# Kernel tuning notes

Measured on AMD Instinct MI355X. Metric: run time of the kernel, lower is better.

The kernel has to match this reference:

```python
import jax, jax.numpy as jnp
import numpy as np

# Config derived from init_kwargs
DIM = 256
DSTATE = 64
DCONV = 3
HEADDIM = 64
CHUNK = 256
NGROUPS = 1
DINNER = int(2.0 * DIM)                 # 512
NHEADS = DINNER // HEADDIM              # 8
CONVDIM = DINNER + 2 * NGROUPS * DSTATE  # 640 (x, B, C share the depthwise conv)
DPROJ = 2 * DINNER + 2 * NGROUPS * DSTATE + NHEADS  # z + xBC + dt


def setup_inputs() -> dict:
    key = jax.random.key(0)
    ks = jax.random.split(key, 8)
    B, H, W = 8, 64, 64
    return dict(
        x=jax.random.normal(ks[0], (B, DIM, H, W), jnp.float32),
        ln_w=jnp.ones((DIM,), jnp.float32),
        ln_b=jnp.zeros((DIM,), jnp.float32),
        in_proj_w=jax.random.normal(ks[1], (DPROJ, DIM), jnp.float32) * 0.02,
        conv_w=jax.random.normal(ks[2], (CONVDIM, 1, DCONV, DCONV), jnp.float32) * 0.1,
        conv_b=jnp.zeros((CONVDIM,), jnp.float32),
        A_log=jnp.log(jax.random.uniform(ks[3], (NHEADS,), jnp.float32, 1.0, 16.0)),
        D=jnp.ones((NHEADS,), jnp.float32),
        dt_bias=jax.random.uniform(ks[4], (NHEADS,), jnp.float32, -2.0, 0.0),
        rms_w=jnp.ones((DINNER,), jnp.float32),
        out_proj_w=jax.random.normal(ks[5], (DIM, DINNER), jnp.float32) * 0.02,
    )


def _ssd(X, dA, Bm, Cm, chunk):
    """Mamba2 SSD chunked parallel scan.
    X:  (b, l, h, p)  inputs already multiplied by dt
    dA: (b, l, h)     dt * A (negative)
    Bm, Cm: (b, l, h, n)
    """
    b, l, h, p = X.shape
    n = Bm.shape[-1]
    c = l // chunk
    q = chunk
    Xc = X.reshape(b, c, q, h, p)
    Bc = Bm.reshape(b, c, q, h, n)
    Cc = Cm.reshape(b, c, q, h, n)
    Ac = dA.reshape(b, c, q, h).transpose(0, 3, 1, 2)            # (b,h,c,q)
    Acs = jnp.cumsum(Ac, axis=-1)                                # (b,h,c,q)
    # intra-chunk (diagonal blocks): causal decay matrix L
    tri = jnp.tril(jnp.ones((q, q), bool))
    Ldec = jnp.where(tri, jnp.exp(Acs[..., :, None] - Acs[..., None, :]), 0.0)
    Y_diag = jnp.einsum('bcqhn,bcshn,bhcqs,bcshp->bcqhp', Cc, Bc, Ldec, Xc)
    # per-chunk final states
    decay_states = jnp.exp(Acs[..., -1:] - Acs)                  # (b,h,c,q)
    states = jnp.einsum('bcqhn,bhcq,bcqhp->bchpn', Bc, decay_states, Xc)
    # inter-chunk recurrence (segment-sum over chunk totals)
    A_last = jnp.pad(Acs[..., -1], ((0, 0), (0, 0), (1, 0)))     # (b,h,c+1)
    ccs = jnp.cumsum(A_last, axis=-1)
    tric = jnp.tril(jnp.ones((c + 1, c + 1), bool))
    decay_chunk = jnp.where(tric, jnp.exp(ccs[..., :, None] - ccs[..., None, :]), 0.0)
    states0 = jnp.concatenate([jnp.zeros_like(states[:, :1]), states], axis=1)
    prev = jnp.einsum('bhzc,bchpn->bzhpn', decay_chunk, states0)[:, :-1]
    # contribution of carried-in state (off-diagonal blocks)
    Y_off = jnp.einsum('bcqhn,bchpn,bhcq->bcqhp', Cc, prev, jnp.exp(Acs))
    return (Y_diag + Y_off).reshape(b, l, h, p)


def _forward(x, ln_w, ln_b, in_proj_w, conv_w, conv_b, A_log, D, dt_bias, rms_w, out_proj_w):
    Bn, Cd, Hh, Ww = x.shape
    L = Hh * Ww
    # LayerNorm over channel dim (channel-first LayerNorm2d)
    mu = jnp.mean(x, axis=1, keepdims=True)
    var = jnp.mean((x - mu) ** 2, axis=1, keepdims=True)
    xn = (x - mu) * jax.lax.rsqrt(var + 1e-5)
    xn = xn * ln_w[None, :, None, None] + ln_b[None, :, None, None]
    # input projection (1x1): -> z | xBC | dt
    zxbcdt = jnp.einsum('bchw,dc->bdhw', xn, in_proj_w)
    z = zxbcdt[:, :DINNER]
    xBC = zxbcdt[:, DINNER:DINNER + CONVDIM]
    dt = zxbcdt[:, DINNER + CONVDIM:]                            # (b, nheads, H, W)
    # depthwise 2D conv + SiLU on xBC
    xBC = jax.lax.conv_general_dilated(
        xBC, conv_w, (1, 1), 'SAME',
        dimension_numbers=('NCHW', 'OIHW', 'NCHW'), feature_group_count=CONVDIM)
    xBC = jax.nn.silu(xBC + conv_b[None, :, None, None])
    # flatten spatial -> sequence, channel-last
    def to_seq(t):
        return t.reshape(Bn, t.shape[1], L).transpose(0, 2, 1)
    xBC, dt, z = to_seq(xBC), to_seq(dt), to_seq(z)
    xs = xBC[..., :DINNER].reshape(Bn, L, NHEADS, HEADDIM)
    Bg = xBC[..., DINNER:DINNER + NGROUPS * DSTATE].reshape(Bn, L, NGROUPS, DSTATE)
    Cg = xBC[..., DINNER + NGROUPS * DSTATE:].reshape(Bn, L, NGROUPS, DSTATE)
    hpg = NHEADS // NGROUPS
    Bm = jnp.repeat(Bg, hpg, axis=2)
    Cm = jnp.repeat(Cg, hpg, axis=2)
    dt = jax.nn.softplus(dt + dt_bias[None, None, :])            # (b, L, nheads)
    A = -jnp.exp(A_log)
    y = _ssd(xs * dt[..., None], dt * A[None, None, :], Bm, Cm, CHUNK)
    y = y + D[None, None, :, None] * xs                          # skip connection
    y = y.reshape(Bn, L, DINNER)
    # gated RMSNorm: norm(y * silu(z)) * w
    y = y * jax.nn.silu(z)
    y = y * jax.lax.rsqrt(jnp.mean(y * y, axis=-1, keepdims=True) + 1e-5) * rms_w
    out = jnp.einsum('bld,cd->blc', y, out_proj_w)
    out = out.transpose(0, 2, 1).reshape(Bn, Cd, Hh, Ww)
    return x + out                                               # residual


def reference(x, ln_w, ln_b, in_proj_w, conv_w, conv_b, A_log, D, dt_bias, rms_w, out_proj_w):
    return _forward(x, ln_w, ln_b, in_proj_w, conv_w, conv_b, A_log, D, dt_bias, rms_w, out_proj_w)
```

## Files before the change

### kernel.cpp

```cpp
#include <hip/hip_runtime.h>
#include <hip/hip_bf16.h>
#include <math.h>

#define DIMC   256
#define LSP    4096
#define BATCH  8
#define DINNER 512
#define NHEADS 8
#define HEADDIM 64
#define DSTATE 64
#define CONVDIM 640
#define DPROJ  1160
#define MPAD   1280
#define CHUNK  256
#define NCHUNK 16

typedef unsigned short u16;
typedef __attribute__((ext_vector_type(8))) unsigned short u16x8;
typedef __attribute__((ext_vector_type(8))) short s16x8;
typedef __attribute__((ext_vector_type(4))) float f32x4;

#define MFMA16(a,b,c) __builtin_amdgcn_mfma_f32_16x16x32_bf16((s16x8)(a),(s16x8)(b),(c),0,0,0)

__device__ __forceinline__ float bf2f(u16 u){ return __uint_as_float(((unsigned int)u)<<16); }
__device__ __forceinline__ u16 f2bf(float f){
  unsigned int x = __float_as_uint(f);
  unsigned int r = (x + 0x7fffu + ((x>>16)&1u)) >> 16;
  return (u16)r;
}
__device__ __forceinline__ float softplusf(float x){ return (x > 20.f) ? x : log1pf(expf(x)); }
__device__ __forceinline__ float siluf(float x){ return x / (1.f + expf(-x)); }

__global__ void convert_w(const float* __restrict__ src, u16* __restrict__ dst,
                          int total, int valid){
  int i = blockIdx.x*256 + threadIdx.x;
  if (i >= total) return;
  dst[i] = (i < valid) ? f2bf(src[i]) : (u16)0;
}

__global__ void convert_w_rms(const float* __restrict__ src, const float* __restrict__ rmsw,
                              u16* __restrict__ dst){
  int i = blockIdx.x*256 + threadIdx.x;
  if (i >= DIMC*DINNER) return;
  dst[i] = f2bf(src[i] * rmsw[i & (DINNER-1)]);
}

__global__ void ln_kernel(const float* __restrict__ X, const float* __restrict__ lnw,
                          const float* __restrict__ lnb, u16* __restrict__ XNT) {
  int pos = blockIdx.x*256 + threadIdx.x;
  int b = pos >> 12, l = pos & (LSP-1);
  const float* xb = X + ((size_t)b*DIMC)*LSP + l;
  float sum=0.f, sq=0.f;
  for (int c=0;c<DIMC;c++){ float v=xb[(size_t)c*LSP]; sum+=v; sq+=v*v; }
  float mu = sum*(1.f/DIMC);
  float var = sq*(1.f/DIMC) - mu*mu;
  float rs = rsqrtf(var + 1e-5f);
  u16* ob = XNT + ((size_t)(b*LSP + l))*DIMC;
  for (int c0=0;c0<DIMC;c0+=8){
    u16x8 v8;
    #pragma unroll
    for(int j=0;j<8;j++){
      float v = xb[(size_t)(c0+j)*LSP];
      v8[j] = f2bf((v-mu)*rs*lnw[c0+j] + lnb[c0+j]);
    }
    *(u16x8*)&ob[c0] = v8;
  }
}

__global__ __launch_bounds__(256,2) void gemm_in_fused(
    const u16* __restrict__ W, const u16* __restrict__ XNT,
    u16* __restrict__ ZT, u16* __restrict__ XBC, u16* __restrict__ DT){
  __shared__ u16 Xs[128][264];
  __shared__ u16 Ws[128][32];
  int tid=threadIdx.x, w=tid>>6, lane=tid&63, l15=lane&15, quad=lane>>4;
  int n0=blockIdx.x*128, mh=blockIdx.y, b=blockIdx.z;
  {
    const u16* src = XNT + ((size_t)(b*LSP + n0))*DIMC;
    #pragma unroll
    for (int i=0;i<16;i++){
      int g = i*256 + tid;
      int row = g>>5, c8 = (g&31)*8;
      *(u16x8*)&Xs[row][c8] = *(const u16x8*)&src[(size_t)row*DIMC + c8];
    }
  }
  for (int pti=0; pti<5; pti++){
    int ptg = mh*5 + pti;
    int m0 = ptg*128;
    f32x4 acc[4][4];
    #pragma unroll
    for(int i=0;i<4;i++)
      #pragma unroll
      for(int j=0;j<4;j++) acc[i][j]=(f32x4){0.f,0.f,0.f,0.f};
    for (int k0=0;k0<DIMC;k0+=32){
      __syncthreads();
      {
        int ch = tid*2;
        int r = ch>>2, o=(ch&3)*8;
        *(u16x8*)&Ws[r][o] = *(const u16x8*)&W[(size_t)(m0+r)*DIMC + k0 + o];
        ch++; r = ch>>2; o=(ch&3)*8;
        *(u16x8*)&Ws[r][o] = *(const u16x8*)&W[(size_t)(m0+r)*DIMC + k0 + o];
      }
      __syncthreads();
      u16x8 af[4], bfr[4];
      if (ptg < 4){
        #pragma unroll
        for(int mt=0;mt<4;mt++) af[mt] = *(const u16x8*)&Xs[(w>>1)*64+mt*16+l15][k0+quad*8];
        #pragma unroll
        for(int nt=0;nt<4;nt++) bfr[nt] = *(const u16x8*)&Ws[(w&1)*64+nt*16+l15][quad*8];
      } else {
        #pragma unroll
        for(int mt=0;mt<4;mt++) af[mt] = *(const u16x8*)&Ws[(w>>1)*64+mt*16+l15][quad*8];
        #pragma unroll
        for(int nt=0;nt<4;nt++) bfr[nt] = *(const u16x8*)&Xs[(w&1)*64+nt*16+l15][k0+quad*8];
      }
      #pragma unroll
      for(int mt=0;mt<4;mt++)
        #pragma unroll
        for(int nt=0;nt<4;nt++)
          acc[mt][nt]=MFMA16(af[mt],bfr[nt],acc[mt][nt]);
    }
    if (ptg < 4){
      #pragma unroll
      for(int mt=0;mt<4;mt++)
        #pragma unroll
        for(int nt=0;nt<4;nt++)
          #pragma unroll
          for(int r=0;r<4;r++){
            int lrow = n0 + (w>>1)*64 + mt*16 + quad*4 + r;
            int dcol = m0 + (w&1)*64 + nt*16 + l15;
            ZT[((size_t)b*LSP + lrow)*DINNER + dcol] = f2bf(acc[mt][nt][r]);
          }
    } else {
      #pragma unroll
      for(int mt=0;mt<4;mt++)
        #pragma unroll
        for(int nt=0;nt<4;nt++)
          #pragma unroll
          for(int r=0;r<4;r++){
            int prow = m0 + (w>>1)*64 + mt*16 + quad*4 + r;
            if (prow>=DPROJ) continue;
            int col = n0 + (w&1)*64 + nt*16 + l15;
            u16 v = f2bf(acc[mt][nt][r]);
            if (prow<DINNER+CONVDIM)  XBC[((size_t)b*CONVDIM+(prow-DINNER))*LSP+col]=v;
            else                      DT[((size_t)b*NHEADS+(prow-DINNER-CONVDIM))*LSP+col]=v;
          }
    }
  }
}

__global__ void gemm_out_mfma(const u16* __restrict__ A, const u16* __restrict__ Bm,
                              const float* __restrict__ Res, float* __restrict__ Out){
  __shared__ u16 As[128][32];
  __shared__ u16 Bs[128][32];
  __shared__ float rinv[128];
  int tid=threadIdx.x, w=tid>>6, lane=tid&63, l15=lane&15, quad=lane>>4;
  int b=blockIdx.z, m0=blockIdx.y*128, n0=blockIdx.x*128;
  const u16* Bb = Bm + ((size_t)b*LSP + n0)*DINNER;
  for (int rr=w; rr<128; rr+=4){
    u16x8 v = *(const u16x8*)&Bb[(size_t)rr*DINNER + lane*8];
    float s=0.f;
    #pragma unroll
    for(int j=0;j<8;j++){ float f=bf2f(v[j]); s+=f*f; }
    #pragma unroll
    for(int o=32;o>0;o>>=1) s += __shfl_xor(s,o,64);
    if (lane==0) rinv[rr] = rsqrtf(s*(1.f/DINNER) + 1e-5f);
  }
  f32x4 acc[4][4];
  #pragma unroll
  for(int i=0;i<4;i++)
    #pragma unroll
    for(int j=0;j<4;j++) acc[i][j] = (f32x4){0.f,0.f,0.f,0.f};
  for (int k0=0;k0<DINNER;k0+=32){
    __syncthreads();
    {
      int ch = tid*2;
      int r = ch>>2, o=(ch&3)*8;
      *(u16x8*)&As[r][o] = *(const u16x8*)&A[(size_t)(m0+r)*DINNER + k0 + o];
      *(u16x8*)&Bs[r][o] = *(const u16x8*)&Bb[(size_t)r*DINNER + k0 + o];
      ch++; r = ch>>2; o=(ch&3)*8;
      *(u16x8*)&As[r][o] = *(const u16x8*)&A[(size_t)(m0+r)*DINNER + k0 + o];
      *(u16x8*)&Bs[r][o] = *(const u16x8*)&Bb[(size_t)r*DINNER + k0 + o];
    }
    __syncthreads();
    u16x8 af[4], bfr[4];
    #pragma unroll
    for(int mt=0;mt<4;mt++) af[mt] = *(const u16x8*)&As[(w>>1)*64+mt*16+l15][quad*8];
    #pragma unroll
    for(int nt=0;nt<4;nt++) bfr[nt] = *(const u16x8*)&Bs[(w&1)*64+nt*16+l15][quad*8];
    #pragma unroll
    for(int mt=0;mt<4;mt++)
      #pragma unroll
      for(int nt=0;nt<4;nt++)
        acc[mt][nt]=MFMA16(af[mt],bfr[nt],acc[mt][nt]);
  }
  #pragma unroll
  for(int mt=0;mt<4;mt++)
    #pragma unroll
    for(int nt=0;nt<4;nt++){
      float rv = rinv[(w&1)*64 + nt*16 + l15];
      #pragma unroll
      for(int r=0;r<4;r++){
        int row = m0 + (w>>1)*64 + mt*16 + quad*4 + r;
        int col = n0 + (w&1)*64 + nt*16 + l15;
        size_t oi = ((size_t)b*DIMC+row)*LSP+col;
        Out[oi] = acc[mt][nt][r]*rv + Res[oi];
      }
    }
}

__global__ void conv_kernel(u16* __restrict__ XBC, const float* __restrict__ CW,
                            const float* __restrict__ CB){
  int ch = blockIdx.x, b = blockIdx.y, tid = threadIdx.x;
  __shared__ float plane[66*66];
  u16* base = XBC + ((size_t)b*CONVDIM + ch)*LSP;
  for (int idx=tid; idx<66*66; idx+=256){
    int yy = idx/66 - 1, xx = idx%66 - 1;
    float v = 0.f;
    if (yy>=0 && yy<64 && xx>=0 && xx<64) v = bf2f(base[yy*64+xx]);
    plane[idx] = v;
  }
  float wg[9];
  #pragma unroll
  for (int t=0;t<9;t++) wg[t] = CW[ch*9+t];
  float bias = CB[ch];
  __syncthreads();
  for (int r=0;r<16;r++){
    int pix = tid + r*256;
    int y = pix>>6, x = pix&63;
    float s=0.f;
    #pragma unroll
    for(int dy=0;dy<3;dy++)
      #pragma unroll
      for(int dx=0;dx<3;dx++) s += plane[(y+dy)*66 + x+dx]*wg[dy*3+dx];
    base[pix] = f2bf(siluf(s + bias));
  }
}

__global__ void ssd_pre_kernel(const u16* __restrict__ DT, const float* __restrict__ A_log,
                               const float* __restrict__ dt_bias, float* __restrict__ ACS,
                               float* __restrict__ DTV, float* __restrict__ DASUM){
  int c=blockIdx.x, h=blockIdx.y, b=blockIdx.z, tid=threadIdx.x;
  __shared__ float acs[CHUNK];
  size_t base = ((size_t)b*NHEADS+h)*LSP + c*CHUNK + tid;
  float raw = bf2f(DT[base]);
  float dtv = softplusf(raw + dt_bias[h]);
  float Ah = -expf(A_log[h]);
  acs[tid] = dtv*Ah;
  __syncthreads();
  for(int o=1;o<256;o<<=1){
    float add=(tid>=o)?acs[tid-o]:0.f;
    __syncthreads(); acs[tid]+=add; __syncthreads();
  }
  ACS[base] = acs[tid];
  DTV[base] = dtv;
  if (tid==CHUNK-1) DASUM[((size_t)b*NHEADS+h)*NCHUNK+c] = acs[tid];
}

__global__ __launch_bounds__(256,4) void ssd_states_mfma(
    const float* __restrict__ ACS, const float* __restrict__ DTV,
    const float* __restrict__ DASUM, const u16* __restrict__ XBC,
    float* __restrict__ STATES){
  int c=blockIdx.x, h=blockIdx.y, b=blockIdx.z;
  int tid=threadIdx.x, w=tid>>6, lane=tid&63, l15=lane&15, quad=lane>>4;
  __shared__ float wdt[CHUNK];
  __shared__ u16 Xw[64][136];
  __shared__ u16 Bn[64][136];
  {
    size_t base = ((size_t)b*NHEADS+h)*LSP + c*CHUNK + tid;
    float atot = DASUM[((size_t)b*NHEADS+h)*NCHUNK+c];
    wdt[tid] = DTV[base]*expf(atot - ACS[base]);
  }
  __syncthreads();
  f32x4 acc[4];
  #pragma unroll
  for(int i=0;i<4;i++) acc[i] = (f32x4){0.f,0.f,0.f,0.f};
  size_t cb = (size_t)c*CHUNK;
  for(int th=0; th<2; th++){
    __syncthreads();
    {
      int n=tid&63, q4=tid>>6;
      const u16* Xg = XBC + ((size_t)b*CONVDIM + h*HEADDIM + n)*LSP + cb + th*128;
      const u16* Bg = XBC + ((size_t)b*CONVDIM + DINNER + n)*LSP + cb + th*128;
      #pragma unroll
      for(int i=0;i<4;i++){
        int o = q4*32+i*8;
        u16x8 v = *(const u16x8*)&Xg[o];
        u16x8 wv;
        #pragma unroll
        for(int j=0;j<8;j++) wv[j]=f2bf(bf2f(v[j])*wdt[th*128+o+j]);
        *(u16x8*)&Xw[n][o]=wv;
        *(u16x8*)&Bn[n][o] = *(const u16x8*)&Bg[o];
      }
    }
    __syncthreads();
    #pragma unroll
    for(int k8=0;k8<4;k8++){
      u16x8 a = *(const u16x8*)&Xw[w*16+l15][k8*32+quad*8];
      #pragma unroll
      for(int nt=0;nt<4;nt++){
        u16x8 bb = *(const u16x8*)&Bn[nt*16+l15][k8*32+quad*8];
        acc[nt]=MFMA16(a,bb,acc[nt]);
      }
    }
  }
  float* dst = STATES + (((size_t)b*NHEADS+h)*NCHUNK+c)*4096;
  #pragma unroll
  for(int nt=0;nt<4;nt++)
    #pragma unroll
    for(int r=0;r<4;r++)
      dst[(w*16+quad*4+r)*64 + nt*16+l15] = acc[nt][r];
}

__global__ void ssd_scan_kernel(const float* __restrict__ STATES, const float* __restrict__ DASUM,
                                u16* __restrict__ PREVB){
  int g = blockIdx.x, h = blockIdx.y, b = blockIdx.z, tid = threadIdx.x;
  int e = g*256 + tid;
  size_t hb = (size_t)b*NHEADS + h;
  size_t base = hb*NCHUNK*4096 + e;
  float s = 0.f;
  for (int cc=0;cc<NCHUNK;cc++){
    PREVB[base + (size_t)cc*4096] = f2bf(s);
    s = s*expf(DASUM[hb*NCHUNK + cc]) + STATES[base + (size_t)cc*4096];
  }
}

__global__ __launch_bounds__(256,4) void ssd_y_mfma(
    const float* __restrict__ ACS, const float* __restrict__ DTV,
    const u16* __restrict__ XBC, const float* __restrict__ Dp,
    const u16* __restrict__ PREVB, const u16* __restrict__ ZT,
    u16* __restrict__ YG){
  int bx = blockIdx.x; int c = bx>>2, tb = bx&3;
  int h = blockIdx.y, b = blockIdx.z;
  int tid=threadIdx.x, w=tid>>6, lane=tid&63, l15=lane&15, quad=lane>>4;
  __shared__ float acs[CHUNK];
  __shared__ float dtv[CHUNK];
  __shared__ u16 Ct[64][72];
  __shared__ u16 Bsb[64][72];
  __shared__ u16 Xsb[64][72];
  __shared__ u16 P[4][16][72];
  {
    size_t base = ((size_t)b*NHEADS+h)*LSP + c*CHUNK + tid;
    acs[tid] = ACS[base];
    dtv[tid] = DTV[base];
  }
  {
    int n = tid&63, q4 = tid>>6;
    const u16* Cg = XBC + ((size_t)b*CONVDIM + DINNER + DSTATE + n)*LSP + (size_t)c*CHUNK + tb*64;
    #pragma unroll
    for(int i=0;i<2;i++){
      u16x8 v = *(const u16x8*)&Cg[q4*16+i*8];
      #pragma unroll
      for(int j=0;j<8;j++) Ct[q4*16+i*8+j][n]=v[j];
    }
  }
  __syncthreads();
  f32x4 Yd[4], Yo[4];
  #pragma unroll
  for(int i=0;i<4;i++){ Yd[i]=(f32x4){0.f,0.f,0.f,0.f}; Yo[i]=(f32x4){0.f,0.f,0.f,0.f}; }
  int trow = w*16 + l15;
  u16x8 ca0 = *(const u16x8*)&Ct[trow][quad*8];
  u16x8 ca1 = *(const u16x8*)&Ct[trow][32+quad*8];
  {
    const u16* Pg = PREVB + (((size_t)b*NHEADS+h)*NCHUNK + c)*4096;
    #pragma unroll
    for(int pt=0;pt<4;pt++){
      u16x8 b0 = *(const u16x8*)&Pg[(pt*16+l15)*64 + quad*8];
      u16x8 b1 = *(const u16x8*)&Pg[(pt*16+l15)*64 + 32 + quad*8];
      Yo[pt]=MFMA16(ca0,b0,Yo[pt]);
      Yo[pt]=MFMA16(ca1,b1,Yo[pt]);
    }
  }
  int tloc = tb*64 + w*16 + quad*4;
  float acst[4];
  #pragma unroll
  for(int r=0;r<4;r++) acst[r] = acs[tloc+r];
  for(int sb=0; sb<=tb; sb++){
    __syncthreads();
    {
      int n=tid&63, q4=tid>>6;
      const u16* Bg = XBC + ((size_t)b*CONVDIM + DINNER + n)*LSP + (size_t)c*CHUNK + sb*64;
      #pragma unroll
      for(int i=0;i<2;i++){
        u16x8 v = *(const u16x8*)&Bg[q4*16+i*8];
        #pragma unroll
        for(int j=0;j<8;j++) Bsb[q4*16+i*8+j][n]=v[j];
      }
      const u16* Xg = XBC + ((size_t)b*CONVDIM + h*HEADDIM + n)*LSP + (size_t)c*CHUNK + sb*64;
      #pragma unroll
      for(int i=0;i<2;i++){
        int o = q4*16+i*8;
        *(u16x8*)&Xsb[n][o] = *(const u16x8*)&Xg[o];
      }
    }
    __syncthreads();
    f32x4 S[4];
    #pragma unroll
    for(int st=0;st<4;st++) S[st]=(f32x4){0.f,0.f,0.f,0.f};
    #pragma unroll
    for(int st=0;st<4;st++){
      u16x8 b0 = *(const u16x8*)&Bsb[st*16+l15][quad*8];
      u16x8 b1 = *(const u16x8*)&Bsb[st*16+l15][32+quad*8];
      S[st]=MFMA16(ca0,b0,S[st]);
      S[st]=MFMA16(ca1,b1,S[st]);
    }
    if (sb < tb){
      #pragma unroll
      for(int st=0;st<4;st++){
        int s = sb*64 + st*16 + l15;
        float as = acs[s];
        float dv = dtv[s];
        #pragma unroll
        for(int r=0;r<4;r++)
          P[w][quad*4+r][st*16+l15] = f2bf(S[st][r]*expf(acst[r]-as)*dv);
      }
    } else {
      #pragma unroll
      for(int st=0;st<4;st++){
        int s = sb*64 + st*16 + l15;
        float as = acs[s];
        float dv = dtv[s];
        #pragma unroll
        for(int r=0;r<4;r++){
          float e = (s <= tloc+r) ? expf(acst[r]-as) : 0.f;
          P[w][quad*4+r][st*16+l15] = f2bf(S[st][r]*e*dv);
        }
      }
    }
    u16x8 p0 = *(const u16x8*)&P[w][l15][quad*8];
    u16x8 p1 = *(const u16x8*)&P[w][l15][32+quad*8];
    #pragma unroll
    for(int pt=0;pt<4;pt++){
      u16x8 x0 = *(const u16x8*)&Xsb[pt*16+l15][quad*8];
      u16x8 x1 = *(const u16x8*)&Xsb[pt*16+l15][32+quad*8];
      Yd[pt]=MFMA16(p0,x0,Yd[pt]);
      Yd[pt]=MFMA16(p1,x1,Yd[pt]);
    }
  }
  float Dh = Dp[h];
  float eat[4];
  #pragma unroll
  for(int r=0;r<4;r++) eat[r] = expf(acst[r]);
  size_t lbase = (size_t)b*LSP + c*CHUNK + tb*64;
  #pragma unroll
  for(int pt=0;pt<4;pt++){
    #pragma unroll
    for(int r=0;r<4;r++){
      int tl = w*16 + quad*4 + r;
      int p = pt*16 + l15;
      float xs = bf2f(Xsb[p][tl]);
      float y = Yd[pt][r] + eat[r]*Yo[pt][r] + Dh*xs;
      size_t oi = (lbase + tl)*DINNER + h*HEADDIM + p;
      float zv = bf2f(ZT[oi]);
      YG[oi] = f2bf(y * siluf(zv));
    }
  }
}

extern "C" void kernel_launch(void* const* d_in, const int* in_sizes, int n_in,
                              void* d_out, int out_size, void* d_ws, size_t ws_size,
                              hipStream_t stream) {
  const float* x     = (const float*)d_in[0];
  const float* lnw   = (const float*)d_in[1];
  const float* lnb   = (const float*)d_in[2];
  const float* inpw  = (const float*)d_in[3];
  const float* convw = (const float*)d_in[4];
  const float* convb = (const float*)d_in[5];
  const float* alog  = (const float*)d_in[6];
  const float* Dp    = (const float*)d_in[7];
  const float* dtbi  = (const float*)d_in[8];
  const float* rmsw  = (const float*)d_in[9];
  const float* outw  = (const float*)d_in[10];
  float* out = (float*)d_out;

  char* ws = (char*)d_ws;
  size_t off = 0;
  auto alloc = [&](size_t bytes)->void*{ void* p = ws+off; off += (bytes+255)&~(size_t)255; return p; };
  u16*   WPIN   = (u16*)  alloc((size_t)MPAD*DIMC*2);
  u16*   WPOUT  = (u16*)  alloc((size_t)DIMC*DINNER*2);
  char*  RA     = (char*) alloc((size_t)BATCH*NHEADS*NCHUNK*4096*4);
  u16*   XNT    = (u16*)RA;
  float* STATES = (float*)RA;
  u16*   ZT     = (u16*)  alloc((size_t)BATCH*LSP*DINNER*2);
  u16*   XBC    = (u16*)  alloc((size_t)BATCH*CONVDIM*LSP*2);
  u16*   DTb    = (u16*)  alloc((size_t)BATCH*NHEADS*LSP*2);
  u16*   PREVB  = (u16*)  alloc((size_t)BATCH*NHEADS*NCHUNK*4096*2);
  float* DASUM  = (float*)alloc((size_t)BATCH*NHEADS*NCHUNK*4);
  float* ACS    = (float*)alloc((size_t)BATCH*NHEADS*LSP*4);
  float* DTV    = (float*)alloc((size_t)BATCH*NHEADS*LSP*4);
  u16*   YG     = (u16*)  alloc((size_t)BATCH*LSP*DINNER*2);

  convert_w<<<(MPAD*DIMC+255)/256,256,0,stream>>>(inpw, WPIN, MPAD*DIMC, DPROJ*DIMC);
  convert_w_rms<<<(DIMC*DINNER+255)/256,256,0,stream>>>(outw, rmsw, WPOUT);
  ln_kernel<<<dim3(BATCH*LSP/256),256,0,stream>>>(x,lnw,lnb,XNT);
  gemm_in_fused<<<dim3(LSP/128,2,BATCH),256,0,stream>>>(WPIN, XNT, ZT, XBC, DTb);
  conv_kernel<<<dim3(CONVDIM,BATCH),256,0,stream>>>(XBC, convw, convb);
  ssd_pre_kernel<<<dim3(NCHUNK,NHEADS,BATCH),256,0,stream>>>(DTb, alog, dtbi, ACS, DTV, DASUM);
  ssd_states_mfma<<<dim3(NCHUNK,NHEADS,BATCH),256,0,stream>>>(ACS,DTV,DASUM,XBC,STATES);
  ssd_scan_kernel<<<dim3(16,NHEADS,BATCH),256,0,stream>>>(STATES,DASUM,PREVB);
  ssd_y_mfma<<<dim3(NCHUNK*4,NHEADS,BATCH),256,0,stream>>>(ACS,DTV,XBC,Dp,PREVB,ZT,YG);
  gemm_out_mfma<<<dim3(LSP/128,DIMC/128,BATCH),256,0,stream>>>(WPOUT, YG, x, out);
}
```

Baseline: 366.0 us.

## Process whole chunk per block in SSD output kernel and use fast math intrinsics

Restructures ssd_y_mfma so that one block handles a full 256-step chunk instead of one 64-row tile. Each B/X sub-block is now loaded once and reused across all later target tiles, rather than being reloaded by every tile block. The D skip term is folded into the diagonal of the decay matrix, and the inter-chunk term is computed by pre-scaling C with exp(acs) into the same accumulators. Softplus, silu and exp now use fast intrinsics (__expf, __logf, rcp). In exchange the kernel launches four times fewer blocks, needs more registers (launch bounds relaxed to 2) and more LDS, and the fast math plus the bf16 pre-scaling reduce precision.

New measurement: 376.2 us. +2.8%, slower.

```diff
diff --git a/kernel.cpp b/kernel.cpp
--- a/kernel.cpp
+++ b/kernel.cpp
@@ -28,8 +28,14 @@
   unsigned int r = (x + 0x7fffu + ((x>>16)&1u)) >> 16;
   return (u16)r;
 }
-__device__ __forceinline__ float softplusf(float x){ return (x > 20.f) ? x : log1pf(expf(x)); }
-__device__ __forceinline__ float siluf(float x){ return x / (1.f + expf(-x)); }
+__device__ __forceinline__ float softplusf(float x){ return (x > 20.f) ? x : __logf(1.f + __expf(x)); }
+__device__ __forceinline__ float siluf(float x){ return x * __builtin_amdgcn_rcpf(1.f + __expf(-x)); }
+__device__ __forceinline__ u16x8 fscale(u16x8 v, float s){
+  u16x8 r;
+  #pragma unroll
+  for(int j=0;j<8;j++) r[j] = f2bf(bf2f(v[j])*s);
+  return r;
+}
 
 __global__ void convert_w(const float* __restrict__ src, u16* __restrict__ dst,
                           int total, int valid){
@@ -244,7 +250,7 @@
   size_t base = ((size_t)b*NHEADS+h)*LSP + c*CHUNK + tid;
   float raw = bf2f(DT[base]);
   float dtv = softplusf(raw + dt_bias[h]);
-  float Ah = -expf(A_log[h]);
+  float Ah = -__expf(A_log[h]);
   acs[tid] = dtv*Ah;
   __syncthreads();
   for(int o=1;o<256;o<<=1){
@@ -268,7 +274,7 @@
   {
     size_t base = ((size_t)b*NHEADS+h)*LSP + c*CHUNK + tid;
     float atot = DASUM[((size_t)b*NHEADS+h)*NCHUNK+c];
-    wdt[tid] = DTV[base]*expf(atot - ACS[base]);
+    wdt[tid] = DTV[base]*__expf(atot - ACS[base]);
   }
   __syncthreads();
   f32x4 acc[4];
@@ -320,21 +326,20 @@
   float s = 0.f;
   for (int cc=0;cc<NCHUNK;cc++){
     PREVB[base + (size_t)cc*4096] = f2bf(s);
-    s = s*expf(DASUM[hb*NCHUNK + cc]) + STATES[base + (size_t)cc*4096];
-  }
-}
-
-__global__ __launch_bounds__(256,4) void ssd_y_mfma(
+    s = s*__expf(DASUM[hb*NCHUNK + cc]) + STATES[base + (size_t)cc*4096];
+  }
+}
+
+__global__ __launch_bounds__(256,2) void ssd_y_mfma(
     const float* __restrict__ ACS, const float* __restrict__ DTV,
     const u16* __restrict__ XBC, const float* __restrict__ Dp,
     const u16* __restrict__ PREVB, const u16* __restrict__ ZT,
     u16* __restrict__ YG){
-  int bx = blockIdx.x; int c = bx>>2, tb = bx&3;
-  int h = blockIdx.y, b = blockIdx.z;
+  int c = blockIdx.x, h = blockIdx.y, b = blockIdx.z;
   int tid=threadIdx.x, w=tid>>6, lane=tid&63, l15=lane&15, quad=lane>>4;
   __shared__ float acs[CHUNK];
   __shared__ float dtv[CHUNK];
-  __shared__ u16 Ct[64][72];
+  __shared__ u16 Ct[256][72];
   __shared__ u16 Bsb[64][72];
   __shared__ u16 Xsb[64][72];
   __shared__ u16 P[4][16][72];
@@ -345,36 +350,44 @@
   }
   {
     int n = tid&63, q4 = tid>>6;
-    const u16* Cg = XBC + ((size_t)b*CONVDIM + DINNER + DSTATE + n)*LSP + (size_t)c*CHUNK + tb*64;
-    #pragma unroll
-    for(int i=0;i<2;i++){
-      u16x8 v = *(const u16x8*)&Cg[q4*16+i*8];
-      #pragma unroll
-      for(int j=0;j<8;j++) Ct[q4*16+i*8+j][n]=v[j];
+    const u16* Cg = XBC + ((size_t)b*CONVDIM + DINNER + DSTATE + n)*LSP + (size_t)c*CHUNK + q4*64;
+    #pragma unroll
+    for(int i=0;i<8;i++){
+      u16x8 v = *(const u16x8*)&Cg[i*8];
+      #pragma unroll
+      for(int j=0;j<8;j++) Ct[q4*64+i*8+j][n]=v[j];
     }
   }
   __syncthreads();
-  f32x4 Yd[4], Yo[4];
-  #pragma unroll
-  for(int i=0;i<4;i++){ Yd[i]=(f32x4){0.f,0.f,0.f,0.f}; Yo[i]=(f32x4){0.f,0.f,0.f,0.f}; }
-  int trow = w*16 + l15;
-  u16x8 ca0 = *(const u16x8*)&Ct[trow][quad*8];
-  u16x8 ca1 = *(const u16x8*)&Ct[trow][32+quad*8];
+  f32x4 Yd[4][4];
+  #pragma unroll
+  for(int t=0;t<4;t++)
+    #pragma unroll
+    for(int p=0;p<4;p++) Yd[t][p]=(f32x4){0.f,0.f,0.f,0.f};
   {
     const u16* Pg = PREVB + (((size_t)b*NHEADS+h)*NCHUNK + c)*4096;
+    u16x8 pb0[4], pb1[4];
     #pragma unroll
     for(int pt=0;pt<4;pt++){
-      u16x8 b0 = *(const u16x8*)&Pg[(pt*16+l15)*64 + quad*8];
-      u16x8 b1 = *(const u16x8*)&Pg[(pt*16+l15)*64 + 32 + quad*8];
-      Yo[pt]=MFMA16(ca0,b0,Yo[pt]);
-      Yo[pt]=MFMA16(ca1,b1,Yo[pt]);
-    }
-  }
-  int tloc = tb*64 + w*16 + quad*4;
-  float acst[4];
-  #pragma unroll
-  for(int r=0;r<4;r++) acst[r] = acs[tloc+r];
-  for(int sb=0; sb<=tb; sb++){
+      pb0[pt] = *(const u16x8*)&Pg[(pt*16+l15)*64 + quad*8];
+      pb1[pt] = *(const u16x8*)&Pg[(pt*16+l15)*64 + 32 + quad*8];
+    }
+    #pragma unroll
+    for(int tb=0;tb<4;tb++){
+      int trow = tb*64 + w*16 + l15;
+      float ea = __expf(acs[trow]);
+      u16x8 a0 = fscale(*(const u16x8*)&Ct[trow][quad*8], ea);
+      u16x8 a1 = fscale(*(const u16x8*)&Ct[trow][32+quad*8], ea);
+      #pragma unroll
+      for(int pt=0;pt<4;pt++){
+        Yd[tb][pt]=MFMA16(a0,pb0[pt],Yd[tb][pt]);
+        Yd[tb][pt]=MFMA16(a1,pb1[pt],Yd[tb][pt]);
+      }
+    }
+  }
+  float Dh = Dp[h];
+  int tw = w*16 + quad*4;
+  for(int sb=0; sb<4; sb++){
     __syncthreads();
     {
       int n=tid&63, q4=tid>>6;
@@ -388,70 +401,77 @@
       const u16* Xg = XBC + ((size_t)b*CONVDIM + h*HEADDIM + n)*LSP + (size_t)c*CHUNK + sb*64;
       #pragma unroll
       for(int i=0;i<2;i++){
-        int o = q4*16+i*8;
+        int o=q4*16+i*8;
         *(u16x8*)&Xsb[n][o] = *(const u16x8*)&Xg[o];
       }
     }
     __syncthreads();
-    f32x4 S[4];
-    #pragma unroll
-    for(int st=0;st<4;st++) S[st]=(f32x4){0.f,0.f,0.f,0.f};
-    #pragma unroll
-    for(int st=0;st<4;st++){
-      u16x8 b0 = *(const u16x8*)&Bsb[st*16+l15][quad*8];
-      u16x8 b1 = *(const u16x8*)&Bsb[st*16+l15][32+quad*8];
-      S[st]=MFMA16(ca0,b0,S[st]);
-      S[st]=MFMA16(ca1,b1,S[st]);
-    }
-    if (sb < tb){
+    for(int tb=sb; tb<4; tb++){
+      int trow = tb*64 + w*16 + l15;
+      u16x8 ca0 = *(const u16x8*)&Ct[trow][quad*8];
+      u16x8 ca1 = *(const u16x8*)&Ct[trow][32+quad*8];
+      f32x4 S[4];
       #pragma unroll
       for(int st=0;st<4;st++){
-        int s = sb*64 + st*16 + l15;
-        float as = acs[s];
-        float dv = dtv[s];
-        #pragma unroll
-        for(int r=0;r<4;r++)
-          P[w][quad*4+r][st*16+l15] = f2bf(S[st][r]*expf(acst[r]-as)*dv);
-      }
-    } else {
-      #pragma unroll
-      for(int st=0;st<4;st++){
-        int s = sb*64 + st*16 + l15;
-        float as = acs[s];
-        float dv = dtv[s];
-        #pragma unroll
-        for(int r=0;r<4;r++){
-          float e = (s <= tloc+r) ? expf(acst[r]-as) : 0.f;
-          P[w][quad*4+r][st*16+l15] = f2bf(S[st][r]*e*dv);
+        S[st]=(f32x4){0.f,0.f,0.f,0.f};
+        u16x8 b0 = *(const u16x8*)&Bsb[st*16+l15][quad*8];
+        u16x8 b1 = *(const u16x8*)&Bsb[st*16+l15][32+quad*8];
+        S[st]=MFMA16(ca0,b0,S[st]);
+        S[st]=MFMA16(ca1,b1,S[st]);
+      }
+      int tloc = tb*64 + tw;
+      float at[4];
+      #pragma unroll
+      for(int r=0;r<4;r++) at[r]=acs[tloc+r];
+      if (tb > sb){
+        #pragma unroll
+        for(int st=0;st<4;st++){
+          int s = sb*64 + st*16 + l15;
+          float as = acs[s], dv = dtv[s];
+          #pragma unroll
+          for(int r=0;r<4;r++)
+            P[w][quad*4+r][st*16+l15] = f2bf(S[st][r]*__expf(at[r]-as)*dv);
         }
-      }
-    }
-    u16x8 p0 = *(const u16x8*)&P[w][l15][quad*8];
-    u16x8 p1 = *(const u16x8*)&P[w][l15][32+quad*8];
+      } else {
+        #pragma unroll
+        for(int st=0;st<4;st++){
+          int s = sb*64 + st*16 + l15;
+          float as = acs[s], dv = dtv[s];
+          #pragma unroll
+          for(int r=0;r<4;r++){
+            int t = tloc + r;
+            float pv;
+            if (s < t)       pv = S[st][r]*__expf(at[r]-as)*dv;
+            else if (s == t) pv = S[st][r]*dv + Dh;
+            else             pv = 0.f;
+            P[w][quad*4+r][st*16+l15] = f2bf(pv);
+          }
+        }
+      }
+      u16x8 p0 = *(const u16x8*)&P[w][l15][quad*8];
+      u16x8 p1 = *(const u16x8*)&P[w][l15][32+quad*8];
+      #pragma unroll
+      for(int pt=0;pt<4;pt++){
+        u16x8 x0 = *(const u16x8*)&Xsb[pt*16+l15][quad*8];
+        u16x8 x1 = *(const u16x8*)&Xsb[pt*16+l15][32+quad*8];
+        Yd[tb][pt]=MFMA16(p0,x0,Yd[tb][pt]);
+        Yd[tb][pt]=MFMA16(p1,x1,Yd[tb][pt]);
+      }
+    }
+  }
+  size_t lchunk = (size_t)b*LSP + c*CHUNK;
+  #pragma unroll
+  for(int tb=0;tb<4;tb++){
     #pragma unroll
     for(int pt=0;pt<4;pt++){
-      u16x8 x0 = *(const u16x8*)&Xsb[pt*16+l15][quad*8];
-      u16x8 x1 = *(const u16x8*)&Xsb[pt*16+l15][32+quad*8];
-      Yd[pt]=MFMA16(p0,x0,Yd[pt]);
-      Yd[pt]=MFMA16(p1,x1,Yd[pt]);
-    }
-  }
-  float Dh = Dp[h];
-  float eat[4];
-  #pragma unroll
-  for(int r=0;r<4;r++) eat[r] = expf(acst[r]);
-  size_t lbase = (size_t)b*LSP + c*CHUNK + tb*64;
-  #pragma unroll
-  for(int pt=0;pt<4;pt++){
-    #pragma unroll
-    for(int r=0;r<4;r++){
-      int tl = w*16 + quad*4 + r;
-      int p = pt*16 + l15;
-      float xs = bf2f(Xsb[p][tl]);
-      float y = Yd[pt][r] + eat[r]*Yo[pt][r] + Dh*xs;
-      size_t oi = (lbase + tl)*DINNER + h*HEADDIM + p;
-      float zv = bf2f(ZT[oi]);
-      YG[oi] = f2bf(y * siluf(zv));
+      #pragma unroll
+      for(int r=0;r<4;r++){
+        int t = tb*64 + tw + r;
+        int p = pt*16 + l15;
+        size_t oi = (lchunk + t)*DINNER + h*HEADDIM + p;
+        float zv = bf2f(ZT[oi]);
+        YG[oi] = f2bf(Yd[tb][pt][r] * siluf(zv));
+      }
     }
   }
 }
@@ -497,6 +517,6 @@
   ssd_pre_kernel<<<dim3(NCHUNK,NHEADS,BATCH),256,0,stream>>>(DTb, alog, dtbi, ACS, DTV, DASUM);
   ssd_states_mfma<<<dim3(NCHUNK,NHEADS,BATCH),256,0,stream>>>(ACS,DTV,DASUM,XBC,STATES);
   ssd_scan_kernel<<<dim3(16,NHEADS,BATCH),256,0,stream>>>(STATES,DASUM,PREVB);
-  ssd_y_mfma<<<dim3(NCHUNK*4,NHEADS,BATCH),256,0,stream>>>(ACS,DTV,XBC,Dp,PREVB,ZT,YG);
+  ssd_y_mfma<<<dim3(NCHUNK,NHEADS,BATCH),256,0,stream>>>(ACS,DTV,XBC,Dp,PREVB,ZT,YG);
   gemm_out_mfma<<<dim3(LSP/128,DIMC/128,BATCH),256,0,stream>>>(WPOUT, YG, x, out);
 }
```
